# Kernel optimization log

Hardware: AMD Instinct MI355X
Metric: run time of the kernel (lower is better)

## Reference

```python
import jax, jax.numpy as jnp
import numpy as np
import math

B, S, D = 4, 2048, 1024
H = 16
DH = D // H  # 64
DFF = 4096
EPS = 1e-5


def layernorm(x, g, b):
    mu = jnp.mean(x, axis=-1, keepdims=True)
    var = jnp.var(x, axis=-1, keepdims=True)
    return (x - mu) * jax.lax.rsqrt(var + EPS) * g + b


def setup_inputs() -> dict:
    key = jax.random.key(0)
    ks = jax.random.split(key, 16)
    s = 0.02
    return {
        "src": jax.random.normal(ks[0], (B, S, D), jnp.float32),
        # per-head q/k/v projections stacked: [H, D, DH]
        "Wq": jax.random.normal(ks[1], (H, D, DH), jnp.float32) * s,
        "bq": jnp.zeros((H, DH), jnp.float32),
        "Wk": jax.random.normal(ks[2], (H, D, DH), jnp.float32) * s,
        "bk": jnp.zeros((H, DH), jnp.float32),
        "Wv": jax.random.normal(ks[3], (H, D, DH), jnp.float32) * s,
        "bv": jnp.zeros((H, DH), jnp.float32),
        "Wo": jax.random.normal(ks[4], (D, D), jnp.float32) * s,
        "bo": jnp.zeros((D,), jnp.float32),
        "ln1_g": jnp.ones((D,), jnp.float32),
        "ln1_b": jnp.zeros((D,), jnp.float32),
        "W1": jax.random.normal(ks[5], (D, DFF), jnp.float32) * s,
        "b1": jnp.zeros((DFF,), jnp.float32),
        "W2": jax.random.normal(ks[6], (DFF, D), jnp.float32) * s,
        "b2": jnp.zeros((D,), jnp.float32),
        "ln2_g": jnp.ones((D,), jnp.float32),
        "ln2_b": jnp.zeros((D,), jnp.float32),
    }


def reference(src, Wq, bq, Wk, bk, Wv, bv, Wo, bo, ln1_g, ln1_b,
              W1, b1, W2, b2, ln2_g, ln2_b):
    # Batched equivalent of the per-head Python loop (no causal mask: mask=False)
    q = jnp.einsum('bsd,hde->bhse', src, Wq) + bq[None, :, None, :]
    k = jnp.einsum('bsd,hde->bhse', src, Wk) + bk[None, :, None, :]
    v = jnp.einsum('bsd,hde->bhse', src, Wv) + bv[None, :, None, :]
    scores = jnp.einsum('bhse,bhte->bhst', q, k) / math.sqrt(DH)
    attn = jax.nn.softmax(scores, axis=-1)
    ctx = jnp.einsum('bhst,bhte->bhse', attn, v)  # [B,H,S,DH]
    # cat over heads on last dim == transpose then merge
    ctx = ctx.transpose(0, 2, 1, 3).reshape(B, S, D)
    attn_out = ctx @ Wo + bo
    x1 = layernorm(attn_out + src, ln1_g, ln1_b)
    ffn = jax.nn.relu(x1 @ W1 + b1) @ W2 + b2
    return layernorm(ffn + x1, ln2_g, ln2_b)
```

## Files before the change

kernel.cpp:

```cpp
#include <hip/hip_runtime.h>
#include <stdint.h>

#define DEV __device__ __forceinline__

typedef float f32x4 __attribute__((ext_vector_type(4)));
typedef float f32x16 __attribute__((ext_vector_type(16)));
typedef __bf16 bf16x8 __attribute__((ext_vector_type(8)));
typedef __bf16 bf16x4 __attribute__((ext_vector_type(4)));
typedef unsigned short u16x4 __attribute__((ext_vector_type(4)));
typedef unsigned short u16x8 __attribute__((ext_vector_type(8)));
typedef unsigned u32x4 __attribute__((ext_vector_type(4)));

DEV unsigned short f2bf(float f) {
  unsigned u = __builtin_bit_cast(unsigned, f);
  u += 0x7fffu + ((u >> 16) & 1u);
  return (unsigned short)(u >> 16);
}
DEV float bf2f(unsigned short h) {
  unsigned u = ((unsigned)h) << 16;
  return __builtin_bit_cast(float, u);
}
DEV unsigned pkbf(float lo, float hi) {
  unsigned r;
  asm("v_cvt_pk_bf16_f32 %0, %1, %2" : "=v"(r) : "v"(lo), "v"(hi));
  return r;
}
DEV void gload_lds16(const void* g, void* l) {
  __builtin_amdgcn_global_load_lds((const __attribute__((address_space(1))) void*)g,
                                   (__attribute__((address_space(3))) void*)l, 16, 0, 0);
}

__global__ void cvt_f32_bf16(const float* __restrict__ in, unsigned short* __restrict__ out, int n) {
  int i = (blockIdx.x * 256 + threadIdx.x) * 4;
  if (i >= n) return;
  f32x4 v = *(const f32x4*)(in + i);
  u16x4 o;
  o[0] = f2bf(v[0]); o[1] = f2bf(v[1]); o[2] = f2bf(v[2]); o[3] = f2bf(v[3]);
  *(u16x4*)(out + i) = o;
}

__global__ void transpose_cvt(const float* __restrict__ src, unsigned short* __restrict__ dst,
                              int R, int C) {
  __shared__ __align__(16) float t[64][65];
  const int tid = threadIdx.x;
  const int r0 = blockIdx.x * 64, c0 = blockIdx.y * 64;
  const int rr = tid >> 2, q = tid & 3;
  const float* s = src + (size_t)(r0 + rr) * C + c0 + q * 16;
#pragma unroll
  for (int j = 0; j < 4; ++j) {
    f32x4 v = *(const f32x4*)(s + j * 4);
    t[rr][q * 16 + j * 4 + 0] = v[0];
    t[rr][q * 16 + j * 4 + 1] = v[1];
    t[rr][q * 16 + j * 4 + 2] = v[2];
    t[rr][q * 16 + j * 4 + 3] = v[3];
  }
  __syncthreads();
  const int cc = tid >> 2, qq = tid & 3;
  unsigned short* o = dst + (size_t)(c0 + cc) * R + r0 + qq * 16;
  u16x8 a, b;
#pragma unroll
  for (int j = 0; j < 8; ++j) {
    a[j] = f2bf(t[qq * 16 + j][cc]);
    b[j] = f2bf(t[qq * 16 + 8 + j][cc]);
  }
  *(u16x8*)o = a;
  *(u16x8*)(o + 8) = b;
}

__global__ void pack_qkv_w(const float* __restrict__ Wq, const float* __restrict__ Wk,
                           const float* __restrict__ Wv, unsigned short* __restrict__ dst) {
  __shared__ __align__(16) float t[64][65];
  const int tid = threadIdx.x;
  const int z = blockIdx.z, part = z >> 4, h = z & 15;
  const float* src = (part == 0 ? Wq : (part == 1 ? Wk : Wv)) + (size_t)h * 65536;
  const int r0 = blockIdx.x * 64;
  const int rr = tid >> 2, q = tid & 3;
  const float* s = src + (size_t)(r0 + rr) * 64 + q * 16;
#pragma unroll
  for (int j = 0; j < 4; ++j) {
    f32x4 v = *(const f32x4*)(s + j * 4);
    t[rr][q * 16 + j * 4 + 0] = v[0];
    t[rr][q * 16 + j * 4 + 1] = v[1];
    t[rr][q * 16 + j * 4 + 2] = v[2];
    t[rr][q * 16 + j * 4 + 3] = v[3];
  }
  __syncthreads();
  const int cc = tid >> 2, qq = tid & 3;
  unsigned short* o = dst + ((size_t)(part * 1024 + h * 64 + cc)) * 1024 + r0 + qq * 16;
  u16x8 a, b;
#pragma unroll
  for (int j = 0; j < 8; ++j) {
    a[j] = f2bf(t[qq * 16 + j][cc]);
    b[j] = f2bf(t[qq * 16 + 8 + j][cc]);
  }
  *(u16x8*)o = a;
  *(u16x8*)(o + 8) = b;
}

__global__ void pack_bias(const float* __restrict__ bq, const float* __restrict__ bk,
                          const float* __restrict__ bv, float* __restrict__ o) {
  int i = blockIdx.x * 256 + threadIdx.x;
  o[i] = i < 1024 ? bq[i] : (i < 2048 ? bk[i - 1024] : bv[i - 2048]);
}

__global__ void vtrans(const unsigned short* __restrict__ v, unsigned short* __restrict__ vt) {
  __shared__ __align__(16) unsigned short t[64][72];
  const int tid = threadIdx.x;
  const int bh = blockIdx.y, s0 = blockIdx.x * 64;
  const int r = tid >> 2, q = (tid & 3) * 16;
  const unsigned short* g = v + ((size_t)bh * 2048 + s0 + r) * 64 + q;
  *(u16x8*)&t[r][q] = *(const u16x8*)g;
  *(u16x8*)&t[r][q + 8] = *(const u16x8*)(g + 8);
  __syncthreads();
  const int d = tid >> 2, qq = (tid & 3) * 16;
  unsigned short* o = vt + ((size_t)bh * 64 + d) * 2048 + s0 + qq;
  u16x8 a, b;
#pragma unroll
  for (int j = 0; j < 8; ++j) {
    a[j] = t[qq + j][d];
    b[j] = t[qq + 8 + j][d];
  }
  *(u16x8*)o = a;
  *(u16x8*)(o + 8) = b;
}

template <int MODE>
__global__ __launch_bounds__(256, 2) void gemm_bt(
    const unsigned short* __restrict__ A, const unsigned short* __restrict__ Bt,
    const float* __restrict__ bias, unsigned short* __restrict__ out,
    unsigned short* __restrict__ qb, unsigned short* __restrict__ kb,
    unsigned short* __restrict__ vb, int M, int N, int K) {
  __shared__ __align__(16) char As[16384];
  __shared__ __align__(16) char Bs[16384];
  const int tid = threadIdx.x;
  const int wave = tid >> 6, lane = tid & 63;
  const int lrow = lane & 15;
  const int kof = (lane >> 4) * 16;
  const int m0 = blockIdx.y * 128, n0 = blockIdx.x * 128;
  const int wm = (wave >> 1) * 64, wn = (wave & 1) * 64;
  const int chunkrow = lane >> 3;
  const int colb0 = (lane & 7) * 16;

  f32x4 acc[4][4] = {};

  for (int k0 = 0; k0 < K; k0 += 64) {
#pragma unroll
    for (int c = 0; c < 4; ++c) {
      const int chunk = wave * 4 + c;
      const int rowA = chunk * 8 + chunkrow;
      const int srcb = colb0 ^ ((rowA & 7) << 4);
      const char* ga = (const char*)A + ((size_t)(m0 + rowA) * K + k0) * 2 + srcb;
      const char* gb = (const char*)Bt + ((size_t)(n0 + rowA) * K + k0) * 2 + srcb;
      gload_lds16(ga, As + chunk * 1024);
      gload_lds16(gb, Bs + chunk * 1024);
    }
    __syncthreads();
#pragma unroll
    for (int kk = 0; kk < 2; ++kk) {
      bf16x8 af[4], bv4[4];
#pragma unroll
      for (int i = 0; i < 4; ++i) {
        const int ra = wm + i * 16 + lrow;
        af[i] = *(const bf16x8*)(As + ra * 128 + ((kk * 64 + kof) ^ ((ra & 7) << 4)));
        const int rb = wn + i * 16 + lrow;
        bv4[i] = *(const bf16x8*)(Bs + rb * 128 + ((kk * 64 + kof) ^ ((rb & 7) << 4)));
      }
#pragma unroll
      for (int mi = 0; mi < 4; ++mi)
#pragma unroll
        for (int ni = 0; ni < 4; ++ni)
          acc[mi][ni] = __builtin_amdgcn_mfma_f32_16x16x32_bf16(af[mi], bv4[ni], acc[mi][ni], 0, 0, 0);
    }
    __syncthreads();
  }

#pragma unroll
  for (int mi = 0; mi < 4; ++mi) {
    const int row = m0 + wm + mi * 16 + ((lane >> 4) << 2);
#pragma unroll
    for (int ni = 0; ni < 4; ++ni) {
      const int col = n0 + wn + ni * 16 + lrow;
      const float bvv = bias[col];
#pragma unroll
      for (int r = 0; r < 4; ++r) {
        float v = acc[mi][ni][r] + bvv;
        if (MODE == 1) v = fmaxf(v, 0.0f);
        const int rr = row + r;
        if constexpr (MODE == 2) {
          const int part = col >> 10, cc = col & 1023, h = cc >> 6, e = cc & 63;
          if (part == 0) v *= 0.18033688011112042f;
          unsigned short* dst = part == 0 ? qb : (part == 1 ? kb : vb);
          dst[(((size_t)((rr >> 11) * 16 + h)) * 2048 + (rr & 2047)) * 64 + e] = f2bf(v);
        } else {
          out[(size_t)rr * N + col] = f2bf(v);
        }
      }
    }
  }
}

__global__ __launch_bounds__(256, 4) void attn_kernel(
    const unsigned short* __restrict__ q_buf, const unsigned short* __restrict__ k_buf,
    const unsigned short* __restrict__ vt_buf, unsigned short* __restrict__ ctx) {
  __shared__ __align__(16) char Ks[2][8192];
  __shared__ __align__(16) char Vs[2][8192];
  const int tid = threadIdx.x, wave = tid >> 6, lane = tid & 63;
  const int wg = (blockIdx.x & 7) * 128 + (blockIdx.x >> 3);
  const int bh = wg >> 4;
  const int q0 = (wg & 15) * 128;
  const int l31 = lane & 31, hi = lane >> 5;

  bf16x8 qf[4];
#pragma unroll
  for (int kk = 0; kk < 4; ++kk)
    qf[kk] = *(const bf16x8*)(q_buf +
        ((size_t)bh * 2048 + q0 + wave * 32 + l31) * 64 + kk * 16 + hi * 8);

  f32x16 acc_o[2] = {};
  float l_reg = 0.f;

  const int stg_r = tid >> 2;
  const int stg_p = (tid & 3) * 16;

  auto stage = [&](int t, int buf) {
#pragma unroll
    for (int i = 0; i < 2; ++i) {
      const int c = i * 256 + wave * 64 + lane;
      const int row = c >> 3;
      const int col = ((c & 7) * 16) ^ ((row & 7) << 4);
      gload_lds16((const char*)k_buf + ((size_t)(bh * 2048 + t * 64 + row)) * 128 + col,
                  &Ks[buf][(i * 256 + wave * 64) * 16]);
      gload_lds16((const char*)vt_buf + ((size_t)(bh * 64 + row)) * 4096 + t * 128 + col,
                  &Vs[buf][(i * 256 + wave * 64) * 16]);
    }
  };

  stage(0, 0);
  for (int t = 0; t < 32; ++t) {
    const int cur = t & 1;
    __syncthreads();
    stage(t < 31 ? t + 1 : 31, cur ^ 1);

    f32x16 sacc[2] = {};
#pragma unroll
    for (int kk = 0; kk < 4; ++kk) {
      bf16x8 kf[2];
#pragma unroll
      for (int mt = 0; mt < 2; ++mt) {
        const int row = mt * 32 + l31;
        kf[mt] = *(const bf16x8*)&Ks[cur][row * 128 + ((kk * 32 + hi * 16) ^ ((row & 7) << 4))];
      }
      __builtin_amdgcn_s_setprio(1);
#pragma unroll
      for (int mt = 0; mt < 2; ++mt)
        sacc[mt] = __builtin_amdgcn_mfma_f32_32x32x16_bf16(kf[mt], qf[kk], sacc[mt], 0, 0, 0);
      __builtin_amdgcn_s_setprio(0);
    }

#pragma unroll
    for (int mt = 0; mt < 2; ++mt)
#pragma unroll
      for (int r = 0; r < 16; ++r)
        sacc[mt][r] = exp2f(sacc[mt][r]);
    {
      f32x4 s0 = {sacc[0][0], sacc[0][1], sacc[0][2], sacc[0][3]};
      f32x4 s1 = {sacc[0][4], sacc[0][5], sacc[0][6], sacc[0][7]};
      f32x4 s2 = {sacc[0][8], sacc[0][9], sacc[0][10], sacc[0][11]};
      f32x4 s3 = {sacc[0][12], sacc[0][13], sacc[0][14], sacc[0][15]};
#pragma unroll
      for (int r = 0; r < 4; ++r) {
        s0[r] += sacc[1][r];  s1[r] += sacc[1][4 + r];
        s2[r] += sacc[1][8 + r];  s3[r] += sacc[1][12 + r];
      }
      f32x4 s01 = s0 + s1, s23 = s2 + s3;
      f32x4 sa = s01 + s23;
      l_reg += (sa[0] + sa[1]) + (sa[2] + sa[3]);
    }

#pragma unroll
    for (int g = 0; g < 4; ++g) {
      const int m = g >> 1, c = g & 1;
      unsigned w0 = pkbf(sacc[m][8 * c + 0], sacc[m][8 * c + 1]);
      unsigned w1 = pkbf(sacc[m][8 * c + 2], sacc[m][8 * c + 3]);
      unsigned w2 = pkbf(sacc[m][8 * c + 4], sacc[m][8 * c + 5]);
      unsigned w3 = pkbf(sacc[m][8 * c + 6], sacc[m][8 * c + 7]);
      u32x4 bw = {w0, w1, w2, w3};
      bf16x8 pb = __builtin_bit_cast(bf16x8, bw);
      bf16x8 vf[2];
#pragma unroll
      for (int mtd = 0; mtd < 2; ++mtd) {
        const int row = mtd * 32 + l31;
        const int cb = g * 32 + hi * 8;
        const int sw = (row & 7) << 4;
        bf16x4 lo = *(const bf16x4*)&Vs[cur][row * 128 + (cb ^ sw)];
        bf16x4 hi4 = *(const bf16x4*)&Vs[cur][row * 128 + ((cb + 16) ^ sw)];
        vf[mtd] = __builtin_shufflevector(lo, hi4, 0, 1, 2, 3, 4, 5, 6, 7);
      }
      __builtin_amdgcn_s_setprio(1);
#pragma unroll
      for (int mtd = 0; mtd < 2; ++mtd)
        acc_o[mtd] = __builtin_amdgcn_mfma_f32_32x32x16_bf16(vf[mtd], pb, acc_o[mtd], 0, 0, 0);
      __builtin_amdgcn_s_setprio(0);
    }
  }

  const float den = l_reg + __shfl_xor(l_reg, 32);
  const float inv = 1.0f / den;
  const int b = bh >> 4, h = bh & 15;
  const size_t orow = ((size_t)(b * 2048 + q0 + wave * 32 + l31)) * 1024 + h * 64;
#pragma unroll
  for (int mtd = 0; mtd < 2; ++mtd)
#pragma unroll
    for (int gq = 0; gq < 4; ++gq) {
      u16x4 o;
#pragma unroll
      for (int e = 0; e < 4; ++e) o[e] = f2bf(acc_o[mtd][gq * 4 + e] * inv);
      *(u16x4*)(ctx + orow + mtd * 32 + gq * 8 + hi * 4) = o;
    }
}

template <bool RES_BF, bool OUT_F32>
__global__ __launch_bounds__(256) void ln_kernel(
    const unsigned short* __restrict__ xin, const void* __restrict__ res,
    const float* __restrict__ g, const float* __restrict__ b, void* __restrict__ out) {
  const int row = blockIdx.x, tid = threadIdx.x;
  const size_t base = (size_t)row * 1024 + tid * 4;
  float x[4];
  u16x4 xv = *(const u16x4*)(xin + base);
  if constexpr (RES_BF) {
    u16x4 rv = *(const u16x4*)((const unsigned short*)res + base);
#pragma unroll
    for (int j = 0; j < 4; ++j) x[j] = bf2f(xv[j]) + bf2f(rv[j]);
  } else {
    f32x4 rv = *(const f32x4*)((const float*)res + base);
#pragma unroll
    for (int j = 0; j < 4; ++j) x[j] = bf2f(xv[j]) + rv[j];
  }
  float s1 = 0.f, s2 = 0.f;
#pragma unroll
  for (int j = 0; j < 4; ++j) { s1 += x[j]; s2 += x[j] * x[j]; }
#pragma unroll
  for (int off = 32; off > 0; off >>= 1) {
    s1 += __shfl_down(s1, off);
    s2 += __shfl_down(s2, off);
  }
  __shared__ float red[8];
  const int wv = tid >> 6, ln = tid & 63;
  if (ln == 0) { red[wv] = s1; red[4 + wv] = s2; }
  __syncthreads();
  s1 = red[0] + red[1] + red[2] + red[3];
  s2 = red[4] + red[5] + red[6] + red[7];
  const float mu = s1 * (1.0f / 1024.0f);
  const float rs = rsqrtf(s2 * (1.0f / 1024.0f) - mu * mu + 1e-5f);
#pragma unroll
  for (int j = 0; j < 4; ++j) {
    const float y = (x[j] - mu) * rs * g[tid * 4 + j] + b[tid * 4 + j];
    if constexpr (OUT_F32) ((float*)out)[base + j] = y;
    else ((unsigned short*)out)[base + j] = f2bf(y);
  }
}

static const size_t OFF_SBF  = 0;
static const size_t OFF_Q    = 16777216;
static const size_t OFF_K    = 33554432;
static const size_t OFF_V    = 50331648;
static const size_t OFF_VT   = 67108864;
static const size_t OFF_WQKV = 83886080;
static const size_t OFF_BQKV = 90177536;
static const size_t OFF_WO   = 90189824;
static const size_t OFF_W1   = 92286976;
static const size_t OFF_W2   = 100675584;
static const size_t OFF_CTX  = 109064192;
static const size_t OFF_AO   = 125841408;
static const size_t OFF_X1   = 142618624;
static const size_t OFF_FFN  = 159395840;

extern "C" void kernel_launch(void* const* d_in, const int* in_sizes, int n_in,
                              void* d_out, int out_size, void* d_ws, size_t ws_size,
                              hipStream_t stream) {
  const float* src = (const float*)d_in[0];
  const float* Wq  = (const float*)d_in[1];
  const float* bq  = (const float*)d_in[2];
  const float* Wk  = (const float*)d_in[3];
  const float* bk  = (const float*)d_in[4];
  const float* Wv  = (const float*)d_in[5];
  const float* bv  = (const float*)d_in[6];
  const float* Wo  = (const float*)d_in[7];
  const float* bo  = (const float*)d_in[8];
  const float* g1  = (const float*)d_in[9];
  const float* be1 = (const float*)d_in[10];
  const float* W1  = (const float*)d_in[11];
  const float* b1  = (const float*)d_in[12];
  const float* W2  = (const float*)d_in[13];
  const float* b2  = (const float*)d_in[14];
  const float* g2  = (const float*)d_in[15];
  const float* be2 = (const float*)d_in[16];

  char* ws = (char*)d_ws;
  unsigned short* sbf  = (unsigned short*)(ws + OFF_SBF);
  unsigned short* h1   = (unsigned short*)(ws + OFF_SBF);
  unsigned short* qb   = (unsigned short*)(ws + OFF_Q);
  unsigned short* kb   = (unsigned short*)(ws + OFF_K);
  unsigned short* vb   = (unsigned short*)(ws + OFF_V);
  unsigned short* vtb  = (unsigned short*)(ws + OFF_VT);
  unsigned short* wqkv = (unsigned short*)(ws + OFF_WQKV);
  float*          bqkv = (float*)(ws + OFF_BQKV);
  unsigned short* wot  = (unsigned short*)(ws + OFF_WO);
  unsigned short* w1t  = (unsigned short*)(ws + OFF_W1);
  unsigned short* w2t  = (unsigned short*)(ws + OFF_W2);
  unsigned short* ctx  = (unsigned short*)(ws + OFF_CTX);
  unsigned short* ao   = (unsigned short*)(ws + OFF_AO);
  unsigned short* x1   = (unsigned short*)(ws + OFF_X1);
  unsigned short* ffn  = (unsigned short*)(ws + OFF_FFN);
  float* outp = (float*)d_out;

  cvt_f32_bf16<<<dim3(8192), dim3(256), 0, stream>>>(src, sbf, 8388608);
  pack_qkv_w<<<dim3(16, 1, 48), dim3(256), 0, stream>>>(Wq, Wk, Wv, wqkv);
  pack_bias<<<dim3(12), dim3(256), 0, stream>>>(bq, bk, bv, bqkv);
  transpose_cvt<<<dim3(16, 16), dim3(256), 0, stream>>>(Wo, wot, 1024, 1024);
  transpose_cvt<<<dim3(16, 64), dim3(256), 0, stream>>>(W1, w1t, 1024, 4096);
  transpose_cvt<<<dim3(64, 16), dim3(256), 0, stream>>>(W2, w2t, 4096, 1024);

  gemm_bt<2><<<dim3(24, 64), dim3(256), 0, stream>>>(sbf, wqkv, bqkv, nullptr, qb, kb, vb,
                                                     8192, 3072, 1024);
  vtrans<<<dim3(32, 64), dim3(256), 0, stream>>>(vb, vtb);
  attn_kernel<<<dim3(1024), dim3(256), 0, stream>>>(qb, kb, vtb, ctx);
  gemm_bt<0><<<dim3(8, 64), dim3(256), 0, stream>>>(ctx, wot, bo, ao, nullptr, nullptr, nullptr,
                                                    8192, 1024, 1024);
  ln_kernel<false, false><<<dim3(8192), dim3(256), 0, stream>>>(ao, src, g1, be1, x1);
  gemm_bt<1><<<dim3(32, 64), dim3(256), 0, stream>>>(x1, w1t, b1, h1, nullptr, nullptr, nullptr,
                                                     8192, 4096, 1024);
  gemm_bt<0><<<dim3(8, 64), dim3(256), 0, stream>>>(h1, w2t, b2, ffn, nullptr, nullptr, nullptr,
                                                    8192, 1024, 4096);
  ln_kernel<true, true><<<dim3(8192), dim3(256), 0, stream>>>(ffn, x1, g2, be2, outp);

  (void)in_sizes; (void)n_in; (void)out_size; (void)ws_size;
}
```

Before: 389.2 us.

## Add 256x256 ping-pong pipelined GEMM for QKV and FFN1 projections

Adds a new 512-thread GEMM kernel with 256x256 output tiles, double-buffered 64 KB LDS stages fed by direct global-to-LDS loads, XOR-swizzled LDS layout, and a barrier-interleaved schedule that alternates LDS reads, async loads and MFMA quarters under raised wave priority. It also remaps workgroup IDs across XCDs. It replaces the 128x128 gemm_bt for the QKV projection and the W1 projection, aiming for more data reuse per tile and overlap of memory with MFMA. The cost is much larger LDS and register use, many barriers, and fewer workgroups per GPU.

```diff
diff --git a/kernel.cpp b/kernel.cpp
--- a/kernel.cpp
+++ b/kernel.cpp
@@ -122,6 +122,155 @@
   }
   *(u16x8*)o = a;
   *(u16x8*)(o + 8) = b;
+}
+
+template <int MODE>
+__global__ __launch_bounds__(512, 2) void gemm8(
+    const unsigned short* __restrict__ A, const unsigned short* __restrict__ Bt,
+    const float* __restrict__ bias, unsigned short* __restrict__ out,
+    unsigned short* __restrict__ qb, unsigned short* __restrict__ kb,
+    unsigned short* __restrict__ vb, int M, int N, int K, int NBN) {
+  __shared__ __align__(16) char As[2][32768];
+  __shared__ __align__(16) char Bs[2][32768];
+  const int tid = threadIdx.x, wave = tid >> 6, lane = tid & 63;
+  const int lrow = lane & 15, lgk = (lane >> 4) * 16;
+  const int cr = lane >> 3;
+  const int csw = ((lane & 7) * 16) ^ (cr << 4);
+  const int nwg = gridDim.x, bid = blockIdx.x;
+  const int wg = (bid & 7) * (nwg >> 3) + (bid >> 3);
+  const int bm = wg / NBN, bn = wg % NBN;
+  const int m0 = bm * 256, n0 = bn * 256;
+  const int wm = (wave >> 2) * 128, wn = (wave & 3) * 64;
+  const char* Ab = (const char*)A;
+  const char* Bb = (const char*)Bt;
+  const int NT = K >> 6;
+
+  f32x4 acc[8][4] = {};
+  bf16x8 af[4][2];
+  bf16x8 bf0[2][2], bf1[2][2];
+
+#define ISSUE_A(kt, half) do {                                                \
+    _Pragma("unroll") for (int rep = 0; rep < 2; ++rep) {                     \
+      const int j = wave * 2 + rep;                                           \
+      const int row0 = j * 8 + ((j >= 8) ? 64 : 0) + (half) * 64;             \
+      gload_lds16(Ab + (((size_t)(m0 + row0 + cr) * K + (kt) * 64) << 1) + csw,\
+                  &As[(kt) & 1][row0 * 128]);                                 \
+    } } while (0)
+#define ISSUE_B(kt, half) do {                                                \
+    _Pragma("unroll") for (int rep = 0; rep < 2; ++rep) {                     \
+      const int j = wave * 2 + rep;                                           \
+      const int row0 = (j >> 2) * 64 + (j & 3) * 8 + (half) * 32;             \
+      gload_lds16(Bb + (((size_t)(n0 + row0 + cr) * K + (kt) * 64) << 1) + csw,\
+                  &Bs[(kt) & 1][row0 * 128]);                                 \
+    } } while (0)
+#define READ_A(dbuf, mh) do {                                                 \
+    _Pragma("unroll") for (int i = 0; i < 4; ++i) {                           \
+      const int row = wm + ((mh) * 4 + i) * 16 + lrow;                        \
+      const int sw = (row & 7) << 4;                                          \
+      af[i][0] = *(const bf16x8*)&As[dbuf][row * 128 + (lgk ^ sw)];           \
+      af[i][1] = *(const bf16x8*)&As[dbuf][row * 128 + ((64 + lgk) ^ sw)];    \
+    } } while (0)
+#define READ_B(dbuf, nh, bfx) do {                                            \
+    _Pragma("unroll") for (int i = 0; i < 2; ++i) {                           \
+      const int row = wn + ((nh) * 2 + i) * 16 + lrow;                        \
+      const int sw = (row & 7) << 4;                                          \
+      bfx[i][0] = *(const bf16x8*)&Bs[dbuf][row * 128 + (lgk ^ sw)];          \
+      bfx[i][1] = *(const bf16x8*)&Bs[dbuf][row * 128 + ((64 + lgk) ^ sw)];   \
+    } } while (0)
+#define MFMA_Q(mh, nh, bfx) do {                                              \
+    __builtin_amdgcn_s_setprio(1);                                            \
+    _Pragma("unroll") for (int i = 0; i < 4; ++i)                             \
+    _Pragma("unroll") for (int n = 0; n < 2; ++n)                             \
+    _Pragma("unroll") for (int kk = 0; kk < 2; ++kk)                          \
+      acc[(mh) * 4 + i][(nh) * 2 + n] = __builtin_amdgcn_mfma_f32_16x16x32_bf16(\
+          af[i][kk], bfx[n][kk], acc[(mh) * 4 + i][(nh) * 2 + n], 0, 0, 0);   \
+    __builtin_amdgcn_s_setprio(0);                                            \
+  } while (0)
+#define BAR() __builtin_amdgcn_s_barrier()
+#define LGKM0() do { asm volatile("s_waitcnt lgkmcnt(0)" ::: "memory");       \
+    __builtin_amdgcn_sched_barrier(0); } while (0)
+#define VMCNT6() asm volatile("s_waitcnt vmcnt(6)" ::: "memory")
+#define VMCNT0() asm volatile("s_waitcnt vmcnt(0)" ::: "memory")
+
+  ISSUE_A(0, 0); ISSUE_B(0, 0); ISSUE_B(0, 1); ISSUE_A(0, 1);
+  __syncthreads();
+  ISSUE_A(1, 0); ISSUE_B(1, 0); ISSUE_B(1, 1);
+
+  for (int a = 0; a < NT; a += 2) {
+    const int d0 = a & 1, d1 = d0 ^ 1;
+    const bool g2 = (a + 2) < NT, g3 = (a + 3) < NT;
+    READ_A(d0, 0); READ_B(d0, 0, bf0);
+    ISSUE_A(a + 1, 1);
+    BAR(); LGKM0();
+    MFMA_Q(0, 0, bf0);
+    BAR();
+    READ_B(d0, 1, bf1);
+    if (g2) ISSUE_A(a + 2, 0);
+    BAR(); LGKM0();
+    MFMA_Q(0, 1, bf1);
+    BAR();
+    READ_A(d0, 1);
+    if (g2) ISSUE_B(a + 2, 0);
+    BAR(); LGKM0();
+    MFMA_Q(1, 0, bf0);
+    BAR();
+    if (g2) { ISSUE_B(a + 2, 1); VMCNT6(); } else { VMCNT0(); }
+    BAR();
+    MFMA_Q(1, 1, bf1);
+    BAR();
+    READ_A(d1, 0); READ_B(d1, 0, bf0);
+    if (g2) ISSUE_A(a + 2, 1);
+    BAR(); LGKM0();
+    MFMA_Q(0, 0, bf0);
+    BAR();
+    READ_B(d1, 1, bf1);
+    if (g3) ISSUE_A(a + 3, 0);
+    BAR(); LGKM0();
+    MFMA_Q(0, 1, bf1);
+    BAR();
+    READ_A(d1, 1);
+    if (g3) ISSUE_B(a + 3, 0);
+    BAR(); LGKM0();
+    MFMA_Q(1, 0, bf0);
+    BAR();
+    if (g3) { ISSUE_B(a + 3, 1); VMCNT6(); } else { VMCNT0(); }
+    BAR();
+    MFMA_Q(1, 1, bf1);
+    BAR();
+  }
+#undef ISSUE_A
+#undef ISSUE_B
+#undef READ_A
+#undef READ_B
+#undef MFMA_Q
+#undef BAR
+#undef LGKM0
+#undef VMCNT6
+#undef VMCNT0
+
+#pragma unroll
+  for (int mi = 0; mi < 8; ++mi) {
+    const int row = m0 + wm + mi * 16 + ((lane >> 4) << 2);
+#pragma unroll
+    for (int ni = 0; ni < 4; ++ni) {
+      const int col = n0 + wn + ni * 16 + lrow;
+      const float bvv = bias[col];
+#pragma unroll
+      for (int r = 0; r < 4; ++r) {
+        float v = acc[mi][ni][r] + bvv;
+        if (MODE == 1) v = fmaxf(v, 0.0f);
+        const int rr = row + r;
+        if constexpr (MODE == 2) {
+          const int part = col >> 10, cc = col & 1023, h = cc >> 6, e = cc & 63;
+          if (part == 0) v *= 0.18033688011112042f;
+          unsigned short* dst = part == 0 ? qb : (part == 1 ? kb : vb);
+          dst[(((size_t)((rr >> 11) * 16 + h)) * 2048 + (rr & 2047)) * 64 + e] = f2bf(v);
+        } else {
+          out[(size_t)rr * N + col] = f2bf(v);
+        }
+      }
+    }
+  }
 }
 
 template <int MODE>
@@ -186,17 +335,11 @@
         float v = acc[mi][ni][r] + bvv;
         if (MODE == 1) v = fmaxf(v, 0.0f);
         const int rr = row + r;
-        if constexpr (MODE == 2) {
-          const int part = col >> 10, cc = col & 1023, h = cc >> 6, e = cc & 63;
-          if (part == 0) v *= 0.18033688011112042f;
-          unsigned short* dst = part == 0 ? qb : (part == 1 ? kb : vb);
-          dst[(((size_t)((rr >> 11) * 16 + h)) * 2048 + (rr & 2047)) * 64 + e] = f2bf(v);
-        } else {
-          out[(size_t)rr * N + col] = f2bf(v);
-        }
+        out[(size_t)rr * N + col] = f2bf(v);
       }
     }
   }
+  (void)qb; (void)kb; (void)vb;
 }
 
 __global__ __launch_bounds__(256, 4) void attn_kernel(
@@ -218,9 +361,6 @@
 
   f32x16 acc_o[2] = {};
   float l_reg = 0.f;
-
-  const int stg_r = tid >> 2;
-  const int stg_p = (tid & 3) * 16;
 
   auto stage = [&](int t, int buf) {
 #pragma unroll
@@ -421,15 +561,15 @@
   transpose_cvt<<<dim3(16, 64), dim3(256), 0, stream>>>(W1, w1t, 1024, 4096);
   transpose_cvt<<<dim3(64, 16), dim3(256), 0, stream>>>(W2, w2t, 4096, 1024);
 
-  gemm_bt<2><<<dim3(24, 64), dim3(256), 0, stream>>>(sbf, wqkv, bqkv, nullptr, qb, kb, vb,
-                                                     8192, 3072, 1024);
+  gemm8<2><<<dim3(384), dim3(512), 0, stream>>>(sbf, wqkv, bqkv, nullptr, qb, kb, vb,
+                                                8192, 3072, 1024, 12);
   vtrans<<<dim3(32, 64), dim3(256), 0, stream>>>(vb, vtb);
   attn_kernel<<<dim3(1024), dim3(256), 0, stream>>>(qb, kb, vtb, ctx);
   gemm_bt<0><<<dim3(8, 64), dim3(256), 0, stream>>>(ctx, wot, bo, ao, nullptr, nullptr, nullptr,
                                                     8192, 1024, 1024);
   ln_kernel<false, false><<<dim3(8192), dim3(256), 0, stream>>>(ao, src, g1, be1, x1);
-  gemm_bt<1><<<dim3(32, 64), dim3(256), 0, stream>>>(x1, w1t, b1, h1, nullptr, nullptr, nullptr,
-                                                     8192, 4096, 1024);
+  gemm8<1><<<dim3(512), dim3(512), 0, stream>>>(x1, w1t, b1, h1, nullptr, nullptr, nullptr,
+                                                8192, 4096, 1024, 16);
   gemm_bt<0><<<dim3(8, 64), dim3(256), 0, stream>>>(h1, w2t, b2, ffn, nullptr, nullptr, nullptr,
                                                     8192, 1024, 4096);
   ln_kernel<true, true><<<dim3(8192), dim3(256), 0, stream>>>(ffn, x1, g2, be2, outp);
```

After: 406.0 us. 1.04x slower.

## Restructure attention to 2 waves with 64 queries each and MFMA row sums

Applied to the files above, without the earlier changes.

The attention kernel drops from 4 waves to 2 waves per block, and each wave now handles two 32-query groups, so every K/V fragment read from LDS feeds twice as many MFMAs. The softmax denominator is now accumulated with an extra MFMA against a ones vector instead of VALU reductions. exp2f is replaced with a raw v_exp_f32, and the V layout is permuted in vtrans so V fragments load as single 8-element reads. Register pressure and accumulator count rise, and occupancy drops to 2 blocks of 128 threads, which may reduce latency hiding.

```diff
diff --git a/kernel.cpp b/kernel.cpp
--- a/kernel.cpp
+++ b/kernel.cpp
@@ -23,6 +23,11 @@
 DEV unsigned pkbf(float lo, float hi) {
   unsigned r;
   asm("v_cvt_pk_bf16_f32 %0, %1, %2" : "=v"(r) : "v"(lo), "v"(hi));
+  return r;
+}
+DEV float fexp2(float x) {
+  float r;
+  asm("v_exp_f32 %0, %1" : "=v"(r) : "v"(x));
   return r;
 }
 DEV void gload_lds16(const void* g, void* l) {
@@ -117,8 +122,9 @@
   u16x8 a, b;
 #pragma unroll
   for (int j = 0; j < 8; ++j) {
-    a[j] = t[qq + j][d];
-    b[j] = t[qq + 8 + j][d];
+    const int sa = (j & 3) | ((j & 4) << 1);
+    a[j] = t[qq + sa][d];
+    b[j] = t[qq + sa + 4][d];
   }
   *(u16x8*)o = a;
   *(u16x8*)(o + 8) = b;
@@ -199,7 +205,7 @@
   }
 }
 
-__global__ __launch_bounds__(256, 4) void attn_kernel(
+__global__ __launch_bounds__(128, 2) void attn_kernel(
     const unsigned short* __restrict__ q_buf, const unsigned short* __restrict__ k_buf,
     const unsigned short* __restrict__ vt_buf, unsigned short* __restrict__ ctx) {
   __shared__ __align__(16) char Ks[2][8192];
@@ -210,28 +216,30 @@
   const int q0 = (wg & 15) * 128;
   const int l31 = lane & 31, hi = lane >> 5;
 
-  bf16x8 qf[4];
-#pragma unroll
-  for (int kk = 0; kk < 4; ++kk)
-    qf[kk] = *(const bf16x8*)(q_buf +
-        ((size_t)bh * 2048 + q0 + wave * 32 + l31) * 64 + kk * 16 + hi * 8);
-
-  f32x16 acc_o[2] = {};
-  float l_reg = 0.f;
-
-  const int stg_r = tid >> 2;
-  const int stg_p = (tid & 3) * 16;
+  bf16x8 qf[2][4];
+#pragma unroll
+  for (int qg = 0; qg < 2; ++qg)
+#pragma unroll
+    for (int kk = 0; kk < 4; ++kk)
+      qf[qg][kk] = *(const bf16x8*)(q_buf +
+          ((size_t)bh * 2048 + q0 + wave * 64 + qg * 32 + l31) * 64 + kk * 16 + hi * 8);
+
+  f32x16 acc_o[2][2] = {};
+  f32x16 accd[2] = {};
+  bf16x8 ones;
+#pragma unroll
+  for (int j = 0; j < 8; ++j) ones[j] = (__bf16)1.0f;
 
   auto stage = [&](int t, int buf) {
 #pragma unroll
-    for (int i = 0; i < 2; ++i) {
-      const int c = i * 256 + wave * 64 + lane;
+    for (int i = 0; i < 4; ++i) {
+      const int c = i * 128 + wave * 64 + lane;
       const int row = c >> 3;
       const int col = ((c & 7) * 16) ^ ((row & 7) << 4);
       gload_lds16((const char*)k_buf + ((size_t)(bh * 2048 + t * 64 + row)) * 128 + col,
-                  &Ks[buf][(i * 256 + wave * 64) * 16]);
+                  &Ks[buf][(i * 128 + wave * 64) * 16]);
       gload_lds16((const char*)vt_buf + ((size_t)(bh * 64 + row)) * 4096 + t * 128 + col,
-                  &Vs[buf][(i * 256 + wave * 64) * 16]);
+                  &Vs[buf][(i * 128 + wave * 64) * 16]);
     }
   };
 
@@ -241,7 +249,7 @@
     __syncthreads();
     stage(t < 31 ? t + 1 : 31, cur ^ 1);
 
-    f32x16 sacc[2] = {};
+    f32x16 sacc[2][2] = {};
 #pragma unroll
     for (int kk = 0; kk < 4; ++kk) {
       bf16x8 kf[2];
@@ -252,71 +260,64 @@
       }
       __builtin_amdgcn_s_setprio(1);
 #pragma unroll
+      for (int qg = 0; qg < 2; ++qg)
+#pragma unroll
+        for (int mt = 0; mt < 2; ++mt)
+          sacc[qg][mt] = __builtin_amdgcn_mfma_f32_32x32x16_bf16(kf[mt], qf[qg][kk], sacc[qg][mt], 0, 0, 0);
+      __builtin_amdgcn_s_setprio(0);
+    }
+
+#pragma unroll
+    for (int qg = 0; qg < 2; ++qg)
+#pragma unroll
       for (int mt = 0; mt < 2; ++mt)
-        sacc[mt] = __builtin_amdgcn_mfma_f32_32x32x16_bf16(kf[mt], qf[kk], sacc[mt], 0, 0, 0);
-      __builtin_amdgcn_s_setprio(0);
-    }
-
-#pragma unroll
-    for (int mt = 0; mt < 2; ++mt)
-#pragma unroll
-      for (int r = 0; r < 16; ++r)
-        sacc[mt][r] = exp2f(sacc[mt][r]);
-    {
-      f32x4 s0 = {sacc[0][0], sacc[0][1], sacc[0][2], sacc[0][3]};
-      f32x4 s1 = {sacc[0][4], sacc[0][5], sacc[0][6], sacc[0][7]};
-      f32x4 s2 = {sacc[0][8], sacc[0][9], sacc[0][10], sacc[0][11]};
-      f32x4 s3 = {sacc[0][12], sacc[0][13], sacc[0][14], sacc[0][15]};
-#pragma unroll
-      for (int r = 0; r < 4; ++r) {
-        s0[r] += sacc[1][r];  s1[r] += sacc[1][4 + r];
-        s2[r] += sacc[1][8 + r];  s3[r] += sacc[1][12 + r];
-      }
-      f32x4 s01 = s0 + s1, s23 = s2 + s3;
-      f32x4 sa = s01 + s23;
-      l_reg += (sa[0] + sa[1]) + (sa[2] + sa[3]);
-    }
+#pragma unroll
+        for (int r = 0; r < 16; ++r)
+          sacc[qg][mt][r] = fexp2(sacc[qg][mt][r]);
 
 #pragma unroll
     for (int g = 0; g < 4; ++g) {
       const int m = g >> 1, c = g & 1;
-      unsigned w0 = pkbf(sacc[m][8 * c + 0], sacc[m][8 * c + 1]);
-      unsigned w1 = pkbf(sacc[m][8 * c + 2], sacc[m][8 * c + 3]);
-      unsigned w2 = pkbf(sacc[m][8 * c + 4], sacc[m][8 * c + 5]);
-      unsigned w3 = pkbf(sacc[m][8 * c + 6], sacc[m][8 * c + 7]);
-      u32x4 bw = {w0, w1, w2, w3};
-      bf16x8 pb = __builtin_bit_cast(bf16x8, bw);
       bf16x8 vf[2];
 #pragma unroll
       for (int mtd = 0; mtd < 2; ++mtd) {
         const int row = mtd * 32 + l31;
-        const int cb = g * 32 + hi * 8;
         const int sw = (row & 7) << 4;
-        bf16x4 lo = *(const bf16x4*)&Vs[cur][row * 128 + (cb ^ sw)];
-        bf16x4 hi4 = *(const bf16x4*)&Vs[cur][row * 128 + ((cb + 16) ^ sw)];
-        vf[mtd] = __builtin_shufflevector(lo, hi4, 0, 1, 2, 3, 4, 5, 6, 7);
-      }
-      __builtin_amdgcn_s_setprio(1);
-#pragma unroll
-      for (int mtd = 0; mtd < 2; ++mtd)
-        acc_o[mtd] = __builtin_amdgcn_mfma_f32_32x32x16_bf16(vf[mtd], pb, acc_o[mtd], 0, 0, 0);
-      __builtin_amdgcn_s_setprio(0);
-    }
-  }
-
-  const float den = l_reg + __shfl_xor(l_reg, 32);
-  const float inv = 1.0f / den;
+        vf[mtd] = *(const bf16x8*)&Vs[cur][row * 128 + ((g * 32 + hi * 16) ^ sw)];
+      }
+#pragma unroll
+      for (int qg = 0; qg < 2; ++qg) {
+        unsigned w0 = pkbf(sacc[qg][m][8 * c + 0], sacc[qg][m][8 * c + 1]);
+        unsigned w1 = pkbf(sacc[qg][m][8 * c + 2], sacc[qg][m][8 * c + 3]);
+        unsigned w2 = pkbf(sacc[qg][m][8 * c + 4], sacc[qg][m][8 * c + 5]);
+        unsigned w3 = pkbf(sacc[qg][m][8 * c + 6], sacc[qg][m][8 * c + 7]);
+        u32x4 bw = {w0, w1, w2, w3};
+        bf16x8 pb = __builtin_bit_cast(bf16x8, bw);
+        __builtin_amdgcn_s_setprio(1);
+        accd[qg] = __builtin_amdgcn_mfma_f32_32x32x16_bf16(ones, pb, accd[qg], 0, 0, 0);
+#pragma unroll
+        for (int mtd = 0; mtd < 2; ++mtd)
+          acc_o[qg][mtd] = __builtin_amdgcn_mfma_f32_32x32x16_bf16(vf[mtd], pb, acc_o[qg][mtd], 0, 0, 0);
+        __builtin_amdgcn_s_setprio(0);
+      }
+    }
+  }
+
   const int b = bh >> 4, h = bh & 15;
-  const size_t orow = ((size_t)(b * 2048 + q0 + wave * 32 + l31)) * 1024 + h * 64;
-#pragma unroll
-  for (int mtd = 0; mtd < 2; ++mtd)
-#pragma unroll
-    for (int gq = 0; gq < 4; ++gq) {
-      u16x4 o;
-#pragma unroll
-      for (int e = 0; e < 4; ++e) o[e] = f2bf(acc_o[mtd][gq * 4 + e] * inv);
-      *(u16x4*)(ctx + orow + mtd * 32 + gq * 8 + hi * 4) = o;
-    }
+#pragma unroll
+  for (int qg = 0; qg < 2; ++qg) {
+    const float inv = 1.0f / accd[qg][0];
+    const size_t orow = ((size_t)(b * 2048 + q0 + wave * 64 + qg * 32 + l31)) * 1024 + h * 64;
+#pragma unroll
+    for (int mtd = 0; mtd < 2; ++mtd)
+#pragma unroll
+      for (int gq = 0; gq < 4; ++gq) {
+        u16x4 o;
+#pragma unroll
+        for (int e = 0; e < 4; ++e) o[e] = f2bf(acc_o[qg][mtd][gq * 4 + e] * inv);
+        *(u16x4*)(ctx + orow + mtd * 32 + gq * 8 + hi * 4) = o;
+      }
+  }
 }
 
 template <bool RES_BF, bool OUT_F32>
@@ -424,7 +425,7 @@
   gemm_bt<2><<<dim3(24, 64), dim3(256), 0, stream>>>(sbf, wqkv, bqkv, nullptr, qb, kb, vb,
                                                      8192, 3072, 1024);
   vtrans<<<dim3(32, 64), dim3(256), 0, stream>>>(vb, vtb);
-  attn_kernel<<<dim3(1024), dim3(256), 0, stream>>>(qb, kb, vtb, ctx);
+  attn_kernel<<<dim3(1024), dim3(128), 0, stream>>>(qb, kb, vtb, ctx);
   gemm_bt<0><<<dim3(8, 64), dim3(256), 0, stream>>>(ctx, wot, bo, ao, nullptr, nullptr, nullptr,
                                                     8192, 1024, 1024);
   ln_kernel<false, false><<<dim3(8192), dim3(256), 0, stream>>>(ao, src, g1, be1, x1);
```

Result: faster. 364.6 us (-6.3%).

## Split attention KV range across two workgroups and combine partial sums

Applied to the files above, without the earlier changes.

The attention kernel now splits each query tile's 2048 keys into two halves handled by separate workgroups, doubling the grid to 2048 blocks. Each half writes an unnormalized bf16 numerator and an fp32 denominator, and a new combine kernel sums them and normalizes. The row-sum is now computed with an extra MFMA against a ones vector instead of VALU reductions, exp2 uses raw v_exp_f32, and V fragment loads become single 16-byte reads with a matching permutation in vtrans. This adds intermediate memory traffic, an extra launch and an extra bf16 rounding of the partial numerators, and it reuses workspace buffers for those partials.

```diff
diff --git a/kernel.cpp b/kernel.cpp
--- a/kernel.cpp
+++ b/kernel.cpp
@@ -23,6 +23,11 @@
 DEV unsigned pkbf(float lo, float hi) {
   unsigned r;
   asm("v_cvt_pk_bf16_f32 %0, %1, %2" : "=v"(r) : "v"(lo), "v"(hi));
+  return r;
+}
+DEV float fexp2(float x) {
+  float r;
+  asm("v_exp_f32 %0, %1" : "=v"(r) : "v"(x));
   return r;
 }
 DEV void gload_lds16(const void* g, void* l) {
@@ -117,8 +122,9 @@
   u16x8 a, b;
 #pragma unroll
   for (int j = 0; j < 8; ++j) {
-    a[j] = t[qq + j][d];
-    b[j] = t[qq + 8 + j][d];
+    const int sa = (j & 3) | ((j & 4) << 1);
+    a[j] = t[qq + sa][d];
+    b[j] = t[qq + sa + 4][d];
   }
   *(u16x8*)o = a;
   *(u16x8*)(o + 8) = b;
@@ -201,13 +207,17 @@
 
 __global__ __launch_bounds__(256, 4) void attn_kernel(
     const unsigned short* __restrict__ q_buf, const unsigned short* __restrict__ k_buf,
-    const unsigned short* __restrict__ vt_buf, unsigned short* __restrict__ ctx) {
+    const unsigned short* __restrict__ vt_buf, unsigned short* __restrict__ num0,
+    unsigned short* __restrict__ num1, float* __restrict__ den) {
   __shared__ __align__(16) char Ks[2][8192];
   __shared__ __align__(16) char Vs[2][8192];
   const int tid = threadIdx.x, wave = tid >> 6, lane = tid & 63;
-  const int wg = (blockIdx.x & 7) * 128 + (blockIdx.x >> 3);
-  const int bh = wg >> 4;
-  const int q0 = (wg & 15) * 128;
+  const int wg = (blockIdx.x & 7) * 256 + (blockIdx.x >> 3);
+  const int bh = wg >> 5;
+  const int rem = wg & 31;
+  const int q0 = (rem >> 1) * 128;
+  const int kvh = rem & 1;
+  const int t0 = kvh * 16;
   const int l31 = lane & 31, hi = lane >> 5;
 
   bf16x8 qf[4];
@@ -217,10 +227,10 @@
         ((size_t)bh * 2048 + q0 + wave * 32 + l31) * 64 + kk * 16 + hi * 8);
 
   f32x16 acc_o[2] = {};
-  float l_reg = 0.f;
-
-  const int stg_r = tid >> 2;
-  const int stg_p = (tid & 3) * 16;
+  f32x16 accd = {};
+  bf16x8 ones;
+#pragma unroll
+  for (int j = 0; j < 8; ++j) ones[j] = (__bf16)1.0f;
 
   auto stage = [&](int t, int buf) {
 #pragma unroll
@@ -235,11 +245,11 @@
     }
   };
 
-  stage(0, 0);
-  for (int t = 0; t < 32; ++t) {
-    const int cur = t & 1;
+  stage(t0, 0);
+  for (int tt = 0; tt < 16; ++tt) {
+    const int cur = tt & 1;
     __syncthreads();
-    stage(t < 31 ? t + 1 : 31, cur ^ 1);
+    stage(tt < 15 ? t0 + tt + 1 : t0 + 15, cur ^ 1);
 
     f32x16 sacc[2] = {};
 #pragma unroll
@@ -261,21 +271,7 @@
     for (int mt = 0; mt < 2; ++mt)
 #pragma unroll
       for (int r = 0; r < 16; ++r)
-        sacc[mt][r] = exp2f(sacc[mt][r]);
-    {
-      f32x4 s0 = {sacc[0][0], sacc[0][1], sacc[0][2], sacc[0][3]};
-      f32x4 s1 = {sacc[0][4], sacc[0][5], sacc[0][6], sacc[0][7]};
-      f32x4 s2 = {sacc[0][8], sacc[0][9], sacc[0][10], sacc[0][11]};
-      f32x4 s3 = {sacc[0][12], sacc[0][13], sacc[0][14], sacc[0][15]};
-#pragma unroll
-      for (int r = 0; r < 4; ++r) {
-        s0[r] += sacc[1][r];  s1[r] += sacc[1][4 + r];
-        s2[r] += sacc[1][8 + r];  s3[r] += sacc[1][12 + r];
-      }
-      f32x4 s01 = s0 + s1, s23 = s2 + s3;
-      f32x4 sa = s01 + s23;
-      l_reg += (sa[0] + sa[1]) + (sa[2] + sa[3]);
-    }
+        sacc[mt][r] = fexp2(sacc[mt][r]);
 
 #pragma unroll
     for (int g = 0; g < 4; ++g) {
@@ -290,13 +286,11 @@
 #pragma unroll
       for (int mtd = 0; mtd < 2; ++mtd) {
         const int row = mtd * 32 + l31;
-        const int cb = g * 32 + hi * 8;
         const int sw = (row & 7) << 4;
-        bf16x4 lo = *(const bf16x4*)&Vs[cur][row * 128 + (cb ^ sw)];
-        bf16x4 hi4 = *(const bf16x4*)&Vs[cur][row * 128 + ((cb + 16) ^ sw)];
-        vf[mtd] = __builtin_shufflevector(lo, hi4, 0, 1, 2, 3, 4, 5, 6, 7);
+        vf[mtd] = *(const bf16x8*)&Vs[cur][row * 128 + ((g * 32 + hi * 16) ^ sw)];
       }
       __builtin_amdgcn_s_setprio(1);
+      accd = __builtin_amdgcn_mfma_f32_32x32x16_bf16(ones, pb, accd, 0, 0, 0);
 #pragma unroll
       for (int mtd = 0; mtd < 2; ++mtd)
         acc_o[mtd] = __builtin_amdgcn_mfma_f32_32x32x16_bf16(vf[mtd], pb, acc_o[mtd], 0, 0, 0);
@@ -304,19 +298,37 @@
     }
   }
 
-  const float den = l_reg + __shfl_xor(l_reg, 32);
-  const float inv = 1.0f / den;
-  const int b = bh >> 4, h = bh & 15;
-  const size_t orow = ((size_t)(b * 2048 + q0 + wave * 32 + l31)) * 1024 + h * 64;
+  unsigned short* nump = kvh ? num1 : num0;
+  const size_t nrow = ((size_t)bh * 2048 + q0 + wave * 32 + l31) * 64;
 #pragma unroll
   for (int mtd = 0; mtd < 2; ++mtd)
 #pragma unroll
     for (int gq = 0; gq < 4; ++gq) {
       u16x4 o;
 #pragma unroll
-      for (int e = 0; e < 4; ++e) o[e] = f2bf(acc_o[mtd][gq * 4 + e] * inv);
-      *(u16x4*)(ctx + orow + mtd * 32 + gq * 8 + hi * 4) = o;
-    }
+      for (int e = 0; e < 4; ++e) o[e] = f2bf(acc_o[mtd][gq * 4 + e]);
+      *(u16x4*)(nump + nrow + mtd * 32 + gq * 8 + hi * 4) = o;
+    }
+  if (hi == 0)
+    den[kvh * 131072 + bh * 2048 + q0 + wave * 32 + l31] = accd[0];
+}
+
+__global__ __launch_bounds__(256) void attn_combine(
+    const unsigned short* __restrict__ num0, const unsigned short* __restrict__ num1,
+    const float* __restrict__ den, unsigned short* __restrict__ ctx) {
+  const int i = blockIdx.x * 256 + threadIdx.x;
+  const size_t base = (size_t)i * 8;
+  const int row = (int)(base >> 6);
+  u16x8 a = *(const u16x8*)(num0 + base);
+  u16x8 b = *(const u16x8*)(num1 + base);
+  const float inv = 1.0f / (den[row] + den[131072 + row]);
+  const int bh = row >> 11, s = row & 2047;
+  const int bb = bh >> 4, h = bh & 15;
+  u16x8 o;
+#pragma unroll
+  for (int j = 0; j < 8; ++j)
+    o[j] = f2bf((bf2f(a[j]) + bf2f(b[j])) * inv);
+  *(u16x8*)(ctx + ((size_t)(bb * 2048 + s)) * 1024 + h * 64 + (int)(base & 63)) = o;
 }
 
 template <bool RES_BF, bool OUT_F32>
@@ -399,11 +411,14 @@
   char* ws = (char*)d_ws;
   unsigned short* sbf  = (unsigned short*)(ws + OFF_SBF);
   unsigned short* h1   = (unsigned short*)(ws + OFF_SBF);
+  unsigned short* num0 = (unsigned short*)(ws + OFF_SBF);
   unsigned short* qb   = (unsigned short*)(ws + OFF_Q);
   unsigned short* kb   = (unsigned short*)(ws + OFF_K);
   unsigned short* vb   = (unsigned short*)(ws + OFF_V);
+  unsigned short* num1 = (unsigned short*)(ws + OFF_V);
   unsigned short* vtb  = (unsigned short*)(ws + OFF_VT);
   unsigned short* wqkv = (unsigned short*)(ws + OFF_WQKV);
+  float*          denb = (float*)(ws + OFF_WQKV);
   float*          bqkv = (float*)(ws + OFF_BQKV);
   unsigned short* wot  = (unsigned short*)(ws + OFF_WO);
   unsigned short* w1t  = (unsigned short*)(ws + OFF_W1);
@@ -424,7 +439,8 @@
   gemm_bt<2><<<dim3(24, 64), dim3(256), 0, stream>>>(sbf, wqkv, bqkv, nullptr, qb, kb, vb,
                                                      8192, 3072, 1024);
   vtrans<<<dim3(32, 64), dim3(256), 0, stream>>>(vb, vtb);
-  attn_kernel<<<dim3(1024), dim3(256), 0, stream>>>(qb, kb, vtb, ctx);
+  attn_kernel<<<dim3(2048), dim3(256), 0, stream>>>(qb, kb, vtb, num0, num1, denb);
+  attn_combine<<<dim3(4096), dim3(256), 0, stream>>>(num0, num1, denb, ctx);
   gemm_bt<0><<<dim3(8, 64), dim3(256), 0, stream>>>(ctx, wot, bo, ao, nullptr, nullptr, nullptr,
                                                     8192, 1024, 1024);
   ln_kernel<false, false><<<dim3(8192), dim3(256), 0, stream>>>(ao, src, g1, be1, x1);
```

Measured after the change: 391.8 us. No clear change (+0.7%).
